# Optimization experiments

Hardware: AMD Instinct MI355X
Metric: run time of the kernel (lower is better)

Reference implementation:

```python
import jax, jax.numpy as jnp
import numpy as np

D = 8      # data dim (output_size)
H = 512    # hidden size
B = 2048   # batch


def _masks(d, in_f, out_f):
    # block-diagonal mask (mask_d) and strictly-lower block mask (mask_o)
    md = np.zeros((out_f, in_f), np.float32)
    mo = np.zeros((out_f, in_f), np.float32)
    for i in range(d):
        md[i * out_f // d:(i + 1) * out_f // d, i * in_f // d:(i + 1) * in_f // d] = 1.0
        mo[i * out_f // d:(i + 1) * out_f // d, :(i + 1) * in_f // d] = 1.0
    return jnp.asarray(md), jnp.asarray(mo - md)


def _masked_linear(x, sld, W, logg, bias, d):
    out_f, in_f = W.shape
    md, mo = _masks(d, in_f, out_f)
    v = jnp.exp(W) * md + W * mo                       # weight-normalized masked weight
    v_norm = jnp.sqrt(jnp.sum(v * v, axis=1, keepdims=True))   # [out,1], L2 over in_features
    w = jnp.exp(logg) * v / v_norm
    out = x @ w.T + bias                               # [B,out]
    ld = logg + W - 0.5 * jnp.log(v_norm ** 2)         # [out,in]
    ob, ib = out_f // d, in_f // d
    # extract diagonal blocks (== tf.boolean_mask with mask_d, row-major)
    blocks = ld.reshape(d, ob, d, ib)[np.arange(d), :, np.arange(d), :]   # [d,ob,ib]
    ld_b = jnp.broadcast_to(blocks[None], (x.shape[0], d, ob, ib))        # tile to batch
    # sum_logdets: [.,d,prev_ob,1] -> transpose -> logsumexp accumulate
    sld = jax.nn.logsumexp(jnp.swapaxes(sld, -1, -2) + ld_b, axis=-1, keepdims=True)
    return out, sld


def _tanh(x, sld):
    ld = -2.0 * (x - jnp.log(2.0) + jax.nn.softplus(-2.0 * x))
    return jnp.tanh(x), sld + ld.reshape(sld.shape)


def _bnaf(x, params):
    d = x.shape[-1]
    sld = jnp.zeros((1, d, 1, 1), x.dtype)
    h = x
    for (W, g, b) in params:
        h, sld = _masked_linear(h, sld, W, g, b, d)
        h, sld = _tanh(h, sld)
    return h, jnp.squeeze(sld, (2, 3))


def setup_inputs() -> dict:
    key = jax.random.key(0)
    ks = jax.random.split(key, 13)
    inp = {"x": jax.random.normal(ks[0], (B, D), jnp.float32)}
    dims = [(D, H), (H, H), (H, H), (H, D)]  # (in_features, out_features)
    for j, (i_f, o_f) in enumerate(dims):
        inp[f"W{j+1}"] = jax.random.normal(ks[1 + 3 * j], (o_f, i_f), jnp.float32) * 0.1
        inp[f"logg{j+1}"] = jnp.log(jax.random.uniform(ks[2 + 3 * j], (o_f, 1), jnp.float32, 1e-3, 1.0))
        inp[f"bias{j+1}"] = jax.random.uniform(ks[3 + 3 * j], (o_f,), jnp.float32, -0.1, 0.1)
    return inp


def reference(x, W1, logg1, bias1, W2, logg2, bias2, W3, logg3, bias3, W4, logg4, bias4):
    params = [(W1, logg1, bias1), (W2, logg2, bias2), (W3, logg3, bias3), (W4, logg4, bias4)]
    return _bnaf(x, params)
```

## Files before the change

### kernel.cpp

```cpp
#include <hip/hip_runtime.h>
#include <hip/hip_bf16.h>
#include <math.h>

typedef unsigned short u16;
typedef short v8s __attribute__((ext_vector_type(8)));
typedef float v4f __attribute__((ext_vector_type(4)));

#define LN2F 0.69314718055994530942f

static constexpr size_t OFF_W1Q = 0;
static constexpr size_t OFF_W2Q = 32768;
static constexpr size_t OFF_W3Q = 557056;
static constexpr size_t OFF_W4Q = 1081344;
static constexpr size_t OFF_M1  = 1097728;
static constexpr size_t OFF_M2  = 1099776;
static constexpr size_t OFF_M3  = 1101824;
static constexpr size_t OFF_M4  = 1103872;
static constexpr size_t OFF_E2  = 1103936;
static constexpr size_t OFF_E3  = 1169472;
static constexpr size_t OFF_E4  = 1235008;

__device__ __forceinline__ u16 f2bf(float f) {
  __hip_bfloat16 h = __float2bfloat16(f);
  return *reinterpret_cast<u16*>(&h);
}
__device__ __forceinline__ float bf2f(u16 u) {
  union { unsigned int i; float f; } x; x.i = ((unsigned int)u) << 16; return x.f;
}

__global__ __launch_bounds__(256) void bnaf_prep(
    const float* __restrict__ W1, const float* __restrict__ lg1,
    const float* __restrict__ W2, const float* __restrict__ lg2,
    const float* __restrict__ W3, const float* __restrict__ lg3,
    const float* __restrict__ W4, const float* __restrict__ lg4,
    char* __restrict__ ws)
{
  const int row = blockIdx.x * 4 + (threadIdx.x >> 6);
  const int lane = threadIdx.x & 63;

  int layer, o, in_f, ibshift, RN;
  const float *W, *lg;
  u16* wq; float* marr; u16* E16 = nullptr; float* E32 = nullptr;
  if (row < 512)       { layer=1; o=row;      in_f=8;   ibshift=0; W=W1; lg=lg1; wq=(u16*)(ws+OFF_W1Q); marr=(float*)(ws+OFF_M1); RN=512; }
  else if (row < 1024) { layer=2; o=row-512;  in_f=512; ibshift=6; W=W2; lg=lg2; wq=(u16*)(ws+OFF_W2Q); marr=(float*)(ws+OFF_M2); E16=(u16*)(ws+OFF_E2); RN=512; }
  else if (row < 1536) { layer=3; o=row-1024; in_f=512; ibshift=6; W=W3; lg=lg3; wq=(u16*)(ws+OFF_W3Q); marr=(float*)(ws+OFF_M3); E16=(u16*)(ws+OFF_E3); RN=512; }
  else                 { layer=4; o=row-1536; in_f=512; ibshift=6; W=W4; lg=lg4; wq=(u16*)(ws+OFF_W4Q); marr=(float*)(ws+OFF_M4); E32=(float*)(ws+OFF_E4); RN=16; }
  const bool zero_row = (layer==4 && o >= 8);
  const int i = (layer==4) ? o : (o >> 6);

  float wr[8], vv[8];
  float acc = 0.f;
  #pragma unroll
  for (int k = 0; k < 8; ++k) {
    int c = lane + 64*k;
    float Wv = (!zero_row && c < in_f) ? W[o*in_f + c] : 0.f;
    wr[k] = Wv;
    int j = c >> ibshift;
    float v = (!zero_row && c < in_f) ? ((j==i) ? __expf(Wv) : (j < i ? Wv : 0.f)) : 0.f;
    vv[k] = v;
    acc += v*v;
  }
  #pragma unroll
  for (int d2 = 1; d2 < 64; d2 <<= 1) acc += __shfl_xor(acc, d2);
  const float vn  = sqrtf(acc);
  const float lvn = __logf(vn);
  const float lgo = zero_row ? 0.f : lg[o];
  const float scale = zero_row ? 0.f : (__expf(lgo) / vn);

  const int CH = (in_f < 32) ? 32 : in_f;
  #pragma unroll
  for (int k = 0; k < 8; ++k) {
    int c = lane + 64*k;
    if (c < CH)
      wq[((size_t)(c >> 5) * RN + o) * 32 + (c & 31)] = f2bf(vv[k] * scale);
  }
  float myldb = -INFINITY; int myjj = -1;
  #pragma unroll
  for (int k = 0; k < 8; ++k) {
    int c = lane + 64*k;
    if (!zero_row && c < in_f && (c >> ibshift) == i) {
      myldb = lgo + wr[k] - lvn;
      myjj  = c - (i << ibshift);
    }
  }
  float mm = myldb;
  #pragma unroll
  for (int d2 = 1; d2 < 64; d2 <<= 1) mm = fmaxf(mm, __shfl_xor(mm, d2));
  if (!zero_row) {
    if (lane == 0) marr[o] = mm;
    if (myjj >= 0) {
      float e = __expf(myldb - mm);
      if (E16) E16[o*64 + myjj] = f2bf(e);
      if (E32) E32[o*64 + myjj] = e;
    }
  }
}


__device__ __forceinline__ void zphase2(const u16* __restrict__ wq, const u16* hA,
                                        int t0, int t1, int K0, int K1,
                                        int c16, int q, v4f acc[2], v8s bp0, v8s bp1) {
  const u16* hrow = hA + c16*520 + q*8;
  const u16* wb0  = wq + ((size_t)(t0*16 + c16))*32 + q*8;
  const u16* wb1  = wq + ((size_t)(t1*16 + c16))*32 + q*8;
  v4f z = {0.f,0.f,0.f,0.f};
  v8s a0 = *(const v8s*)(hrow);
  acc[0] = __builtin_amdgcn_mfma_f32_16x16x32_bf16(a0, bp0, z, 0, 0, 0);
  acc[1] = __builtin_amdgcn_mfma_f32_16x16x32_bf16(a0, bp1, z, 0, 0, 0);
  int kt = 1;
  for (; kt < K0; ++kt) {
    v8s a  = *(const v8s*)(hrow + kt*32);
    v8s b0 = *(const v8s*)(wb0 + (size_t)kt*512*32);
    v8s b1 = *(const v8s*)(wb1 + (size_t)kt*512*32);
    acc[0] = __builtin_amdgcn_mfma_f32_16x16x32_bf16(a, b0, acc[0], 0, 0, 0);
    acc[1] = __builtin_amdgcn_mfma_f32_16x16x32_bf16(a, b1, acc[1], 0, 0, 0);
  }
  for (; kt < K1; ++kt) {
    v8s a  = *(const v8s*)(hrow + kt*32);
    v8s b1 = *(const v8s*)(wb1 + (size_t)kt*512*32);
    acc[1] = __builtin_amdgcn_mfma_f32_16x16x32_bf16(a, b1, acc[1], 0, 0, 0);
  }
}

__device__ __forceinline__ void zpost2(const v4f* acc, float bi0, float bi1,
                                       int t0, int t1, int c16, int q,
                                       u16* hout, float tld[2][4]) {
  const float bi[2] = {bi0, bi1};
  const int   tt[2] = {t0, t1};
  #pragma unroll
  for (int s = 0; s < 2; ++s) {
    int o = tt[s]*16 + c16;
    #pragma unroll
    for (int rg = 0; rg < 4; ++rg) {
      float z  = acc[s][rg] + bi[s];
      float t2 = 2.f*z;
      float e2 = __expf(-fabsf(t2));
      float th = copysignf(__fdividef(1.f - e2, 1.f + e2), z);
      float sp = fmaxf(-t2, 0.f) + __logf(1.f + e2);
      tld[s][rg] = -t2 + 2.f*LN2F - 2.f*sp;
      hout[(q*4 + rg)*520 + o] = f2bf(th);
    }
  }
}

__global__ __launch_bounds__(1024) void bnaf_main(
    const float* __restrict__ x,
    const float* __restrict__ b1, const float* __restrict__ b2,
    const float* __restrict__ b3, const float* __restrict__ b4,
    const char* __restrict__ ws, float* __restrict__ out)
{
  __shared__ u16 hA0[16*520];
  __shared__ u16 hA1[16*520];
  __shared__ u16 sexp_s[8*16*64];

  float* pacc = (float*)hA0;
  float* tld4 = (float*)hA1;

  const u16* w1q = (const u16*)(ws + OFF_W1Q);
  const u16* w2q = (const u16*)(ws + OFF_W2Q);
  const u16* w3q = (const u16*)(ws + OFF_W3Q);
  const u16* w4q = (const u16*)(ws + OFF_W4Q);
  const float* m1 = (const float*)(ws + OFF_M1);
  const float* m2 = (const float*)(ws + OFF_M2);
  const float* m3 = (const float*)(ws + OFF_M3);
  const float* m4 = (const float*)(ws + OFF_M4);
  const u16* E2 = (const u16*)(ws + OFF_E2);
  const u16* E3 = (const u16*)(ws + OFF_E3);
  const float* E4 = (const float*)(ws + OFF_E4);

  const int tid = threadIdx.x;
  const int wv = tid >> 6, lane = tid & 63;
  const int c16 = lane & 15, q = lane >> 4;
  const int r0 = blockIdx.x * 16;
  const int t0 = wv, t1 = 31 - wv;
  const int blk0 = wv >> 2, blk1 = 7 - blk0;
  const int K0 = 2*(blk0 + 1), K1 = 2*(blk1 + 1);

  v8s b1p0 = *(const v8s*)(w1q + ((size_t)(t0*16 + c16))*32 + q*8);
  v8s b1p1 = *(const v8s*)(w1q + ((size_t)(t1*16 + c16))*32 + q*8);
  float m1v0 = m1[t0*16 + c16], m1v1 = m1[t1*16 + c16];
  float b1v0 = b1[t0*16 + c16], b1v1 = b1[t1*16 + c16];

  if (tid < 512) {
    int r = tid >> 5, c = tid & 31;
    hA0[r*520 + c] = f2bf((c < 8) ? x[(r0 + r)*8 + c] : 0.f);
  }
  __syncthreads();

  v4f acc[2];
  float tld[2][4], sld[2][4];

  { v8s a = *(const v8s*)(hA0 + c16*520 + q*8);
    v4f z = {0.f,0.f,0.f,0.f};
    acc[0] = __builtin_amdgcn_mfma_f32_16x16x32_bf16(a, b1p0, z, 0, 0, 0);
    acc[1] = __builtin_amdgcn_mfma_f32_16x16x32_bf16(a, b1p1, z, 0, 0, 0); }
  v8s bp0 = *(const v8s*)(w2q + ((size_t)(t0*16 + c16))*32 + q*8);
  v8s bp1 = *(const v8s*)(w2q + ((size_t)(t1*16 + c16))*32 + q*8);
  zpost2(acc, b1v0, b1v1, t0, t1, c16, q, hA1, tld);
  #pragma unroll
  for (int rg = 0; rg < 4; ++rg) {
    sld[0][rg] = m1v0 + tld[0][rg];
    sld[1][rg] = m1v1 + tld[1][rg];
  }
  __syncthreads();

  {
    v8s e00 = *(const v8s*)(E2 + (size_t)(t0*16+c16)*64 + q*8);
    v8s e01 = *(const v8s*)(E2 + (size_t)(t0*16+c16)*64 + 32 + q*8);
    v8s e10 = *(const v8s*)(E2 + (size_t)(t1*16+c16)*64 + q*8);
    v8s e11 = *(const v8s*)(E2 + (size_t)(t1*16+c16)*64 + 32 + q*8);
    float mv0 = m2[t0*16+c16], mv1 = m2[t1*16+c16];
    float bv0 = b2[t0*16+c16], bv1 = b2[t1*16+c16];
    zphase2(w2q, hA1, t0, t1, K0, K1, c16, q, acc, bp0, bp1);
    bp0 = *(const v8s*)(w3q + ((size_t)(t0*16 + c16))*32 + q*8);
    bp1 = *(const v8s*)(w3q + ((size_t)(t1*16 + c16))*32 + q*8);
    zpost2(acc, bv0, bv1, t0, t1, c16, q, hA0, tld);
    #pragma unroll
    for (int rg = 0; rg < 4; ++rg) {
      sexp_s[blk0*1024 + (q*4+rg)*64 + (t0&3)*16 + c16] = f2bf(__expf(sld[0][rg]));
      sexp_s[blk1*1024 + (q*4+rg)*64 + (t1&3)*16 + c16] = f2bf(__expf(sld[1][rg]));
    }
    __syncthreads();
    v4f ea0 = {0.f,0.f,0.f,0.f}, ea1 = {0.f,0.f,0.f,0.f};
    { v8s a0 = *(const v8s*)(sexp_s + blk0*1024 + c16*64 + q*8);
      v8s a1 = *(const v8s*)(sexp_s + blk1*1024 + c16*64 + q*8);
      ea0 = __builtin_amdgcn_mfma_f32_16x16x32_bf16(a0, e00, ea0, 0, 0, 0);
      ea1 = __builtin_amdgcn_mfma_f32_16x16x32_bf16(a1, e10, ea1, 0, 0, 0);
      a0 = *(const v8s*)(sexp_s + blk0*1024 + c16*64 + 32 + q*8);
      a1 = *(const v8s*)(sexp_s + blk1*1024 + c16*64 + 32 + q*8);
      ea0 = __builtin_amdgcn_mfma_f32_16x16x32_bf16(a0, e01, ea0, 0, 0, 0);
      ea1 = __builtin_amdgcn_mfma_f32_16x16x32_bf16(a1, e11, ea1, 0, 0, 0); }
    #pragma unroll
    for (int rg = 0; rg < 4; ++rg) {
      sld[0][rg] = mv0 + __logf(ea0[rg]) + tld[0][rg];
      sld[1][rg] = mv1 + __logf(ea1[rg]) + tld[1][rg];
    }
  }

  v8s bw4;
  {
    v8s e00 = *(const v8s*)(E3 + (size_t)(t0*16+c16)*64 + q*8);
    v8s e01 = *(const v8s*)(E3 + (size_t)(t0*16+c16)*64 + 32 + q*8);
    v8s e10 = *(const v8s*)(E3 + (size_t)(t1*16+c16)*64 + q*8);
    v8s e11 = *(const v8s*)(E3 + (size_t)(t1*16+c16)*64 + 32 + q*8);
    float mv0 = m3[t0*16+c16], mv1 = m3[t1*16+c16];
    float bv0 = b3[t0*16+c16], bv1 = b3[t1*16+c16];
    zphase2(w3q, hA0, t0, t1, K0, K1, c16, q, acc, bp0, bp1);
    bw4 = *(const v8s*)(w4q + ((size_t)(wv*16 + c16))*32 + q*8);
    zpost2(acc, bv0, bv1, t0, t1, c16, q, hA1, tld);
    __syncthreads();
    #pragma unroll
    for (int rg = 0; rg < 4; ++rg) {
      sexp_s[blk0*1024 + (q*4+rg)*64 + (t0&3)*16 + c16] = f2bf(__expf(sld[0][rg]));
      sexp_s[blk1*1024 + (q*4+rg)*64 + (t1&3)*16 + c16] = f2bf(__expf(sld[1][rg]));
    }
    __syncthreads();
    v4f ea0 = {0.f,0.f,0.f,0.f}, ea1 = {0.f,0.f,0.f,0.f};
    { v8s a0 = *(const v8s*)(sexp_s + blk0*1024 + c16*64 + q*8);
      v8s a1 = *(const v8s*)(sexp_s + blk1*1024 + c16*64 + q*8);
      ea0 = __builtin_amdgcn_mfma_f32_16x16x32_bf16(a0, e00, ea0, 0, 0, 0);
      ea1 = __builtin_amdgcn_mfma_f32_16x16x32_bf16(a1, e10, ea1, 0, 0, 0);
      a0 = *(const v8s*)(sexp_s + blk0*1024 + c16*64 + 32 + q*8);
      a1 = *(const v8s*)(sexp_s + blk1*1024 + c16*64 + 32 + q*8);
      ea0 = __builtin_amdgcn_mfma_f32_16x16x32_bf16(a0, e01, ea0, 0, 0, 0);
      ea1 = __builtin_amdgcn_mfma_f32_16x16x32_bf16(a1, e11, ea1, 0, 0, 0); }
    #pragma unroll
    for (int rg = 0; rg < 4; ++rg) {
      sld[0][rg] = mv0 + __logf(ea0[rg]) + tld[0][rg];
      sld[1][rg] = mv1 + __logf(ea1[rg]) + tld[1][rg];
    }
  }

  { v8s a = *(const v8s*)(hA1 + c16*520 + wv*32 + q*8);
    v4f z = {0.f,0.f,0.f,0.f};
    v4f z4 = __builtin_amdgcn_mfma_f32_16x16x32_bf16(a, bw4, z, 0, 0, 0);
    *(v4f*)(pacc + wv*256 + lane*4) = z4; }
  __syncthreads();

  #pragma unroll
  for (int rg = 0; rg < 4; ++rg) {
    sexp_s[blk0*1024 + (q*4+rg)*64 + (t0&3)*16 + c16] = f2bf(__expf(sld[0][rg]));
    sexp_s[blk1*1024 + (q*4+rg)*64 + (t1&3)*16 + c16] = f2bf(__expf(sld[1][rg]));
  }
  if (tid < 256) {
    int s = tid, rg = s & 3, l = s >> 2;
    int c = l & 15, qq = l >> 4, r = qq*4 + rg;
    float z = 0.f;
    #pragma unroll
    for (int w = 0; w < 16; ++w) z += pacc[w*256 + s];
    if (c < 8) {
      z += b4[c];
      float t2 = 2.f*z;
      float e2 = __expf(-fabsf(t2));
      float th = copysignf(__fdividef(1.f - e2, 1.f + e2), z);
      float sp = fmaxf(-t2, 0.f) + __logf(1.f + e2);
      tld4[r*8 + c] = -t2 + 2.f*LN2F - 2.f*sp;
      out[(r0 + r)*8 + c] = th;
    }
  }
  __syncthreads();

  if (wv < 8) {
    int r = c16, i = wv;
    float sum = 0.f;
    #pragma unroll
    for (int jj = 0; jj < 16; ++jj) {
      int j = q*16 + jj;
      sum += bf2f(sexp_s[i*1024 + r*64 + j]) * E4[i*64 + j];
    }
    sum += __shfl_xor(sum, 16);
    sum += __shfl_xor(sum, 32);
    float sldf = m4[i] + __logf(sum) + tld4[r*8 + i];
    if (lane < 16) out[2048*8 + (r0 + r)*8 + i] = sldf;
  }
}

extern "C" void kernel_launch(void* const* d_in, const int* in_sizes, int n_in,
                              void* d_out, int out_size, void* d_ws, size_t ws_size,
                              hipStream_t stream) {
  const float* x   = (const float*)d_in[0];
  const float* W1  = (const float*)d_in[1];
  const float* lg1 = (const float*)d_in[2];
  const float* b1  = (const float*)d_in[3];
  const float* W2  = (const float*)d_in[4];
  const float* lg2 = (const float*)d_in[5];
  const float* b2  = (const float*)d_in[6];
  const float* W3  = (const float*)d_in[7];
  const float* lg3 = (const float*)d_in[8];
  const float* b3  = (const float*)d_in[9];
  const float* W4  = (const float*)d_in[10];
  const float* lg4 = (const float*)d_in[11];
  const float* b4  = (const float*)d_in[12];
  char* ws = (char*)d_ws;
  float* out = (float*)d_out;

  bnaf_prep<<<388, 256, 0, stream>>>(W1, lg1, W2, lg2, W3, lg3, W4, lg4, ws);
  bnaf_main<<<128, 1024, 0, stream>>>(x, b1, b2, b3, b4, ws, out);
}
```

Before: 103.1 us.

## Fuse weight-prep and main kernels into one cooperative launch with grid sync

Merges the weight-normalization prep kernel into the main kernel. Each wave of the 128 blocks processes one weight row, then a cooperative grid-wide sync runs before the MLP/logdet phase. This removes a separate kernel launch and the gap between the two kernels. In exchange it adds a grid barrier and a cooperative launch, and prep now uses only 128 blocks instead of 388.

```diff
diff --git a/kernel.cpp b/kernel.cpp
--- a/kernel.cpp
+++ b/kernel.cpp
@@ -1,6 +1,9 @@
 #include <hip/hip_runtime.h>
 #include <hip/hip_bf16.h>
+#include <hip/hip_cooperative_groups.h>
 #include <math.h>
+
+namespace cg = cooperative_groups;
 
 typedef unsigned short u16;
 typedef short v8s __attribute__((ext_vector_type(8)));
@@ -27,75 +30,6 @@
 __device__ __forceinline__ float bf2f(u16 u) {
   union { unsigned int i; float f; } x; x.i = ((unsigned int)u) << 16; return x.f;
 }
-
-__global__ __launch_bounds__(256) void bnaf_prep(
-    const float* __restrict__ W1, const float* __restrict__ lg1,
-    const float* __restrict__ W2, const float* __restrict__ lg2,
-    const float* __restrict__ W3, const float* __restrict__ lg3,
-    const float* __restrict__ W4, const float* __restrict__ lg4,
-    char* __restrict__ ws)
-{
-  const int row = blockIdx.x * 4 + (threadIdx.x >> 6);
-  const int lane = threadIdx.x & 63;
-
-  int layer, o, in_f, ibshift, RN;
-  const float *W, *lg;
-  u16* wq; float* marr; u16* E16 = nullptr; float* E32 = nullptr;
-  if (row < 512)       { layer=1; o=row;      in_f=8;   ibshift=0; W=W1; lg=lg1; wq=(u16*)(ws+OFF_W1Q); marr=(float*)(ws+OFF_M1); RN=512; }
-  else if (row < 1024) { layer=2; o=row-512;  in_f=512; ibshift=6; W=W2; lg=lg2; wq=(u16*)(ws+OFF_W2Q); marr=(float*)(ws+OFF_M2); E16=(u16*)(ws+OFF_E2); RN=512; }
-  else if (row < 1536) { layer=3; o=row-1024; in_f=512; ibshift=6; W=W3; lg=lg3; wq=(u16*)(ws+OFF_W3Q); marr=(float*)(ws+OFF_M3); E16=(u16*)(ws+OFF_E3); RN=512; }
-  else                 { layer=4; o=row-1536; in_f=512; ibshift=6; W=W4; lg=lg4; wq=(u16*)(ws+OFF_W4Q); marr=(float*)(ws+OFF_M4); E32=(float*)(ws+OFF_E4); RN=16; }
-  const bool zero_row = (layer==4 && o >= 8);
-  const int i = (layer==4) ? o : (o >> 6);
-
-  float wr[8], vv[8];
-  float acc = 0.f;
-  #pragma unroll
-  for (int k = 0; k < 8; ++k) {
-    int c = lane + 64*k;
-    float Wv = (!zero_row && c < in_f) ? W[o*in_f + c] : 0.f;
-    wr[k] = Wv;
-    int j = c >> ibshift;
-    float v = (!zero_row && c < in_f) ? ((j==i) ? __expf(Wv) : (j < i ? Wv : 0.f)) : 0.f;
-    vv[k] = v;
-    acc += v*v;
-  }
-  #pragma unroll
-  for (int d2 = 1; d2 < 64; d2 <<= 1) acc += __shfl_xor(acc, d2);
-  const float vn  = sqrtf(acc);
-  const float lvn = __logf(vn);
-  const float lgo = zero_row ? 0.f : lg[o];
-  const float scale = zero_row ? 0.f : (__expf(lgo) / vn);
-
-  const int CH = (in_f < 32) ? 32 : in_f;
-  #pragma unroll
-  for (int k = 0; k < 8; ++k) {
-    int c = lane + 64*k;
-    if (c < CH)
-      wq[((size_t)(c >> 5) * RN + o) * 32 + (c & 31)] = f2bf(vv[k] * scale);
-  }
-  float myldb = -INFINITY; int myjj = -1;
-  #pragma unroll
-  for (int k = 0; k < 8; ++k) {
-    int c = lane + 64*k;
-    if (!zero_row && c < in_f && (c >> ibshift) == i) {
-      myldb = lgo + wr[k] - lvn;
-      myjj  = c - (i << ibshift);
-    }
-  }
-  float mm = myldb;
-  #pragma unroll
-  for (int d2 = 1; d2 < 64; d2 <<= 1) mm = fmaxf(mm, __shfl_xor(mm, d2));
-  if (!zero_row) {
-    if (lane == 0) marr[o] = mm;
-    if (myjj >= 0) {
-      float e = __expf(myldb - mm);
-      if (E16) E16[o*64 + myjj] = f2bf(e);
-      if (E32) E32[o*64 + myjj] = e;
-    }
-  }
-}
-
 
 __device__ __forceinline__ void zphase2(const u16* __restrict__ wq, const u16* hA,
                                         int t0, int t1, int K0, int K1,
@@ -143,11 +77,13 @@
   }
 }
 
-__global__ __launch_bounds__(1024) void bnaf_main(
+__global__ __launch_bounds__(1024) void bnaf_fused(
     const float* __restrict__ x,
-    const float* __restrict__ b1, const float* __restrict__ b2,
-    const float* __restrict__ b3, const float* __restrict__ b4,
-    const char* __restrict__ ws, float* __restrict__ out)
+    const float* __restrict__ W1, const float* __restrict__ lg1, const float* __restrict__ b1,
+    const float* __restrict__ W2, const float* __restrict__ lg2, const float* __restrict__ b2,
+    const float* __restrict__ W3, const float* __restrict__ lg3, const float* __restrict__ b3,
+    const float* __restrict__ W4, const float* __restrict__ lg4, const float* __restrict__ b4,
+    char* __restrict__ ws, float* __restrict__ out)
 {
   __shared__ u16 hA0[16*520];
   __shared__ u16 hA1[16*520];
@@ -155,23 +91,92 @@
 
   float* pacc = (float*)hA0;
   float* tld4 = (float*)hA1;
+
+  const int tid = threadIdx.x;
+  const int wv = tid >> 6, lane = tid & 63;
+  const int c16 = lane & 15, q = lane >> 4;
+  const int r0 = blockIdx.x * 16;
+
+  if (tid < 512) {
+    int r = tid >> 5, c = tid & 31;
+    hA0[r*520 + c] = f2bf((c < 8) ? x[(r0 + r)*8 + c] : 0.f);
+  }
+
+  {
+    const int row = wv * 128 + blockIdx.x;
+    if (row < 1552) {
+      int layer, o, in_f, ibshift, RN;
+      const float *W, *lg;
+      u16* wq; float* marr; u16* E16 = nullptr; float* E32 = nullptr;
+      if (row < 512)       { layer=1; o=row;      in_f=8;   ibshift=0; W=W1; lg=lg1; wq=(u16*)(ws+OFF_W1Q); marr=(float*)(ws+OFF_M1); RN=512; }
+      else if (row < 1024) { layer=2; o=row-512;  in_f=512; ibshift=6; W=W2; lg=lg2; wq=(u16*)(ws+OFF_W2Q); marr=(float*)(ws+OFF_M2); E16=(u16*)(ws+OFF_E2); RN=512; }
+      else if (row < 1536) { layer=3; o=row-1024; in_f=512; ibshift=6; W=W3; lg=lg3; wq=(u16*)(ws+OFF_W3Q); marr=(float*)(ws+OFF_M3); E16=(u16*)(ws+OFF_E3); RN=512; }
+      else                 { layer=4; o=row-1536; in_f=512; ibshift=6; W=W4; lg=lg4; wq=(u16*)(ws+OFF_W4Q); marr=(float*)(ws+OFF_M4); E32=(float*)(ws+OFF_E4); RN=16; }
+      const bool zero_row = (layer==4 && o >= 8);
+      const int i = (layer==4) ? o : (o >> 6);
+
+      float wr[8], vv[8];
+      float acc = 0.f;
+      #pragma unroll
+      for (int k = 0; k < 8; ++k) {
+        int c = lane + 64*k;
+        float Wv = (!zero_row && c < in_f) ? W[o*in_f + c] : 0.f;
+        wr[k] = Wv;
+        int j = c >> ibshift;
+        float v = (!zero_row && c < in_f) ? ((j==i) ? __expf(Wv) : (j < i ? Wv : 0.f)) : 0.f;
+        vv[k] = v;
+        acc += v*v;
+      }
+      #pragma unroll
+      for (int d2 = 1; d2 < 64; d2 <<= 1) acc += __shfl_xor(acc, d2);
+      const float vn  = sqrtf(acc);
+      const float lvn = __logf(vn);
+      const float lgo = zero_row ? 0.f : lg[o];
+      const float scale = zero_row ? 0.f : (__expf(lgo) / vn);
+
+      const int CH = (in_f < 32) ? 32 : in_f;
+      #pragma unroll
+      for (int k = 0; k < 8; ++k) {
+        int c = lane + 64*k;
+        if (c < CH)
+          wq[((size_t)(c >> 5) * RN + o) * 32 + (c & 31)] = f2bf(vv[k] * scale);
+      }
+      float myldb = -INFINITY; int myjj = -1;
+      #pragma unroll
+      for (int k = 0; k < 8; ++k) {
+        int c = lane + 64*k;
+        if (!zero_row && c < in_f && (c >> ibshift) == i) {
+          myldb = lgo + wr[k] - lvn;
+          myjj  = c - (i << ibshift);
+        }
+      }
+      float mm = myldb;
+      #pragma unroll
+      for (int d2 = 1; d2 < 64; d2 <<= 1) mm = fmaxf(mm, __shfl_xor(mm, d2));
+      if (!zero_row) {
+        if (lane == 0) marr[o] = mm;
+        if (myjj >= 0) {
+          float e = __expf(myldb - mm);
+          if (E16) E16[o*64 + myjj] = f2bf(e);
+          if (E32) E32[o*64 + myjj] = e;
+        }
+      }
+    }
+  }
+
+  __threadfence();
+  cg::this_grid().sync();
 
   const u16* w1q = (const u16*)(ws + OFF_W1Q);
   const u16* w2q = (const u16*)(ws + OFF_W2Q);
   const u16* w3q = (const u16*)(ws + OFF_W3Q);
   const u16* w4q = (const u16*)(ws + OFF_W4Q);
   const float* m1 = (const float*)(ws + OFF_M1);
-  const float* m2 = (const float*)(ws + OFF_M2);
   const float* m3 = (const float*)(ws + OFF_M3);
   const float* m4 = (const float*)(ws + OFF_M4);
-  const u16* E2 = (const u16*)(ws + OFF_E2);
   const u16* E3 = (const u16*)(ws + OFF_E3);
   const float* E4 = (const float*)(ws + OFF_E4);
 
-  const int tid = threadIdx.x;
-  const int wv = tid >> 6, lane = tid & 63;
-  const int c16 = lane & 15, q = lane >> 4;
-  const int r0 = blockIdx.x * 16;
   const int t0 = wv, t1 = 31 - wv;
   const int blk0 = wv >> 2, blk1 = 7 - blk0;
   const int K0 = 2*(blk0 + 1), K1 = 2*(blk1 + 1);
@@ -180,12 +185,6 @@
   v8s b1p1 = *(const v8s*)(w1q + ((size_t)(t1*16 + c16))*32 + q*8);
   float m1v0 = m1[t0*16 + c16], m1v1 = m1[t1*16 + c16];
   float b1v0 = b1[t0*16 + c16], b1v1 = b1[t1*16 + c16];
-
-  if (tid < 512) {
-    int r = tid >> 5, c = tid & 31;
-    hA0[r*520 + c] = f2bf((c < 8) ? x[(r0 + r)*8 + c] : 0.f);
-  }
-  __syncthreads();
 
   v4f acc[2];
   float tld[2][4], sld[2][4];
@@ -205,6 +204,8 @@
   __syncthreads();
 
   {
+    const u16* E2 = (const u16*)(ws + OFF_E2);
+    const float* m2 = (const float*)(ws + OFF_M2);
     v8s e00 = *(const v8s*)(E2 + (size_t)(t0*16+c16)*64 + q*8);
     v8s e01 = *(const v8s*)(E2 + (size_t)(t0*16+c16)*64 + 32 + q*8);
     v8s e10 = *(const v8s*)(E2 + (size_t)(t1*16+c16)*64 + q*8);
@@ -334,6 +335,14 @@
   char* ws = (char*)d_ws;
   float* out = (float*)d_out;
 
-  bnaf_prep<<<388, 256, 0, stream>>>(W1, lg1, W2, lg2, W3, lg3, W4, lg4, ws);
-  bnaf_main<<<128, 1024, 0, stream>>>(x, b1, b2, b3, b4, ws, out);
-}
+  void* args[] = {
+    (void*)&x,
+    (void*)&W1, (void*)&lg1, (void*)&b1,
+    (void*)&W2, (void*)&lg2, (void*)&b2,
+    (void*)&W3, (void*)&lg3, (void*)&b3,
+    (void*)&W4, (void*)&lg4, (void*)&b4,
+    (void*)&ws, (void*)&out
+  };
+  hipLaunchCooperativeKernel((const void*)bnaf_fused, dim3(128), dim3(1024),
+                             args, 0, stream);
+}
```

New measurement: 185.4 us. 79.9% more time.
